# Performance work log

Hardware: AMD Instinct MI355X
Metric: run time of the kernel (lower is better)

Reference implementation:

```python
import jax, jax.numpy as jnp
import numpy as np

NUM_LEVELS = 16
MIN_RES = 16
GROWTH = 1.38
TABLE_SZ = 16384
# Per-level resolutions computed in float64 like torch's python-float b**level
RESOLUTIONS = jnp.asarray(np.floor(MIN_RES * GROWTH ** np.arange(NUM_LEVELS)).astype(np.float32))
# Spatial-hash constants; 2654435761 wraps to int32 like torch's .int() arithmetic
H2 = np.uint32(2654435761).astype(np.int32)
H3 = np.int32(805459861)
# Corner order v0..v7 from get_nearest_vertices_coords: 1 -> use ceil, 0 -> use floor
CORNERS = np.array([[0,0,0],[1,0,0],[1,1,0],[0,1,0],[0,0,1],[1,0,1],[1,1,1],[0,1,1]], dtype=bool)


def setup_inputs() -> dict:
    key = jax.random.key(0)
    kx, kt = jax.random.split(key)
    x = jax.random.uniform(kx, (262144, 3), dtype=jnp.float32)
    # original init: uniform(-1e-4, 1e-4); small-scale random values
    tables = jax.random.normal(kt, (NUM_LEVELS, TABLE_SZ, 2), dtype=jnp.float32) * 1e-4
    return {"x": x, "tables": tables}


def reference(x, tables):
    B = x.shape[0]
    F = tables.shape[-1]
    mask = jnp.asarray(CORNERS)  # [8,3]
    scaled = RESOLUTIONS[:, None, None] * x[None]        # [L,B,3]
    lo = jnp.floor(scaled).astype(jnp.int32)             # [L,B,3]
    hi = jnp.ceil(scaled).astype(jnp.int32)              # [L,B,3]
    verts = jnp.where(mask[None, None], hi[:, :, None, :], lo[:, :, None, :])  # [L,B,8,3]
    vx, vy, vz = verts[..., 0], verts[..., 1], verts[..., 2]
    # int32 spatial hash with wraparound multiply, then python-style mod (non-negative)
    idx = jnp.remainder(vx ^ (H2 * vy) ^ (H3 * vz), TABLE_SZ)  # [L,B,8]
    feats = jax.vmap(lambda t, i: t[i])(tables, idx)           # [L,B,8,F]
    # NOTE: faithful to source: interpolation weights use the UNSCALED position
    w = x - jnp.floor(x)                                       # [B,3]
    # trilinear weight per corner = prod_d (w_d if corner high else 1-w_d)
    cw = jnp.prod(jnp.where(mask[None], w[:, None, :], 1.0 - w[:, None, :]), axis=-1)  # [B,8]
    out = jnp.einsum('lbvf,bv->lbf', feats, cw)                # [L,B,F]
    return jnp.transpose(out, (1, 0, 2)).reshape(B, NUM_LEVELS * F)
```

## Files before the change

### kernel.cpp

```cpp
#include <hip/hip_runtime.h>
#include <hip/hip_fp16.h>
#include <stdint.h>


#define NUM_LEVELS 16
#define TABLE_SZ   16384
#define NCHUNK     32
#define BLOCK      512
#define TBLOCK     256

__constant__ float RESV[NUM_LEVELS] = {
    16.f, 22.f, 30.f, 42.f, 58.f, 80.f, 110.f, 152.f,
    210.f, 290.f, 400.f, 553.f, 763.f, 1053.f, 1453.f, 2005.f
};

struct PointCtx {
    uint32_t off[8];
    float    cw[8];
};

__device__ __forceinline__ void make_ctx(float px, float py, float pz, float r,
                                         PointCtx& c)
{
    float wx = px - floorf(px);
    float wy = py - floorf(py);
    float wz = pz - floorf(pz);
    float ox = 1.f - wx, oy = 1.f - wy, oz = 1.f - wz;

    c.cw[0] = ox * oy * oz;
    c.cw[1] = wx * oy * oz;
    c.cw[2] = wx * wy * oz;
    c.cw[3] = ox * wy * oz;
    c.cw[4] = ox * oy * wz;
    c.cw[5] = wx * oy * wz;
    c.cw[6] = wx * wy * wz;
    c.cw[7] = ox * wy * wz;

    float sx = r * px, sy = r * py, sz = r * pz;
    uint32_t mxl = ((uint32_t)(int)floorf(sx) & (TABLE_SZ - 1)) << 2;
    uint32_t mxh = ((uint32_t)(int)ceilf(sx)  & (TABLE_SZ - 1)) << 2;
    uint32_t myl = ((2654435761u * (uint32_t)(int)floorf(sy)) & (TABLE_SZ - 1)) << 2;
    uint32_t myh = ((2654435761u * (uint32_t)(int)ceilf(sy))  & (TABLE_SZ - 1)) << 2;
    uint32_t mzl = ((805459861u  * (uint32_t)(int)floorf(sz)) & (TABLE_SZ - 1)) << 2;
    uint32_t mzh = ((805459861u  * (uint32_t)(int)ceilf(sz))  & (TABLE_SZ - 1)) << 2;

    c.off[0] = mxl ^ myl ^ mzl;
    c.off[1] = mxh ^ myl ^ mzl;
    c.off[2] = mxh ^ myh ^ mzl;
    c.off[3] = mxl ^ myh ^ mzl;
    c.off[4] = mxl ^ myl ^ mzh;
    c.off[5] = mxh ^ myl ^ mzh;
    c.off[6] = mxh ^ myh ^ mzh;
    c.off[7] = mxl ^ myh ^ mzh;
}

template<int MODE>
__global__ __launch_bounds__(BLOCK, 4)
void hashenc_lds_kernel(const float* __restrict__ x,
                        const float* __restrict__ tables,
                        __half2* __restrict__ ws,
                        float* __restrict__ out,
                        int B, int pts_per_block)
{
    __shared__ __half2 tab[TABLE_SZ];

    const int level = blockIdx.x >> 5;
    const int chunk = blockIdx.x & (NCHUNK - 1);

    {
        const float4* __restrict__ gt4 =
            (const float4*)(tables + (size_t)level * (TABLE_SZ * 2));
        #pragma unroll
        for (int i = threadIdx.x; i < TABLE_SZ / 2; i += BLOCK) {
            float4 v = gt4[i];
            tab[2 * i]     = __floats2half2_rn(v.x, v.y);
            tab[2 * i + 1] = __floats2half2_rn(v.z, v.w);
        }
    }
    __syncthreads();

    const float r = RESV[level];
    const char* tb = (const char*)tab;
    __half2* wsl = ws + (size_t)level * B;

    int b = chunk * pts_per_block + threadIdx.x;
    const int pair_iters = pts_per_block / (2 * BLOCK);

    float pxA = x[3 * b + 0],           pyA = x[3 * b + 1],           pzA = x[3 * b + 2];
    float pxB = x[3 * (b + BLOCK) + 0], pyB = x[3 * (b + BLOCK) + 1], pzB = x[3 * (b + BLOCK) + 2];

    for (int k = 0; k < pair_iters; ++k) {
        float nxA = pxA, nyA = pyA, nzA = pzA;
        float nxB = pxB, nyB = pyB, nzB = pzB;
        int nb = b + 2 * BLOCK;
        if (k + 1 < pair_iters) {
            nxA = x[3 * nb + 0];             nyA = x[3 * nb + 1];             nzA = x[3 * nb + 2];
            nxB = x[3 * (nb + BLOCK) + 0];   nyB = x[3 * (nb + BLOCK) + 1];   nzB = x[3 * (nb + BLOCK) + 2];
        }

        PointCtx cA, cB;
        make_ctx(pxA, pyA, pzA, r, cA);
        make_ctx(pxB, pyB, pzB, r, cB);

        float2 fA[8], fB[8];
        #pragma unroll
        for (int c = 0; c < 8; ++c)
            fA[c] = __half22float2(*(const __half2*)(tb + cA.off[c]));
        #pragma unroll
        for (int c = 0; c < 8; ++c)
            fB[c] = __half22float2(*(const __half2*)(tb + cB.off[c]));

        float a0 = 0.f, a1 = 0.f, b0 = 0.f, b1 = 0.f;
        #pragma unroll
        for (int c = 0; c < 8; ++c) {
            a0 += fA[c].x * cA.cw[c];
            a1 += fA[c].y * cA.cw[c];
            b0 += fB[c].x * cB.cw[c];
            b1 += fB[c].y * cB.cw[c];
        }

        if (MODE == 0) {
            wsl[b]         = __floats2half2_rn(a0, a1);
            wsl[b + BLOCK] = __floats2half2_rn(b0, b1);
        } else {
            ((float2*)out)[(size_t)b * NUM_LEVELS + level]           = make_float2(a0, a1);
            ((float2*)out)[(size_t)(b + BLOCK) * NUM_LEVELS + level] = make_float2(b0, b1);
        }

        pxA = nxA; pyA = nyA; pzA = nzA;
        pxB = nxB; pyB = nyB; pzB = nzB;
        b = nb;
    }
}

__global__ __launch_bounds__(TBLOCK)
void transpose_kernel(const __half2* __restrict__ ws,
                      float* __restrict__ out, int B)
{
    __shared__ __half2 buf[TBLOCK][NUM_LEVELS + 1];
    const int p0 = blockIdx.x * TBLOCK;
    const int t  = threadIdx.x;

    #pragma unroll
    for (int l = 0; l < NUM_LEVELS; ++l)
        buf[t][l] = ws[(size_t)l * B + p0 + t];
    __syncthreads();

    const int pl = t >> 3;
    const int j  = t & 7;
    float4* o = (float4*)out;
    #pragma unroll
    for (int i = 0; i < 8; ++i) {
        int p = pl + i * 32;
        float2 f0 = __half22float2(buf[p][2 * j]);
        float2 f1 = __half22float2(buf[p][2 * j + 1]);
        o[(size_t)(p0 + p) * 8 + j] = make_float4(f0.x, f0.y, f1.x, f1.y);
    }
}

extern "C" void kernel_launch(void* const* d_in, const int* in_sizes, int n_in,
                              void* d_out, int out_size, void* d_ws, size_t ws_size,
                              hipStream_t stream) {
    const float* x      = (const float*)d_in[0];
    const float* tables = (const float*)d_in[1];
    float* out          = (float*)d_out;
    int B = in_sizes[0] / 3;
    int pts_per_block = (B + NCHUNK - 1) / NCHUNK;
    dim3 grid(NUM_LEVELS * NCHUNK);

    size_t ws_needed = (size_t)NUM_LEVELS * B * sizeof(__half2);
    if (ws_size >= ws_needed && (B % TBLOCK) == 0) {
        __half2* ws = (__half2*)d_ws;
        hashenc_lds_kernel<0><<<grid, BLOCK, 0, stream>>>(x, tables, ws, out, B, pts_per_block);
        transpose_kernel<<<dim3(B / TBLOCK), TBLOCK, 0, stream>>>(ws, out, B);
    } else {
        hashenc_lds_kernel<1><<<grid, BLOCK, 0, stream>>>(x, tables, nullptr, out, B, pts_per_block);
    }
}
```

Baseline: 91.95 us.

## Add prep pass converting tables to fp16 and x to SoA; async LDS fill

A new prep kernel converts the hash tables to half2 and splits x into separate x/y/z arrays once, so each of the 512 main blocks fills its LDS table with direct global-to-LDS loads of half-size data instead of loading fp32 and converting. The main loop reads coordinates with coalesced SoA loads instead of strided AoS loads, and the software prefetch of the next point pair is removed. The cost is an extra kernel launch plus workspace traffic for the converted table and the coordinates, and a stricter shape condition before falling back.

```diff
diff --git a/kernel.cpp b/kernel.cpp
--- a/kernel.cpp
+++ b/kernel.cpp
@@ -54,49 +54,69 @@
     c.off[7] = mxl ^ myh ^ mzh;
 }
 
-template<int MODE>
+__global__ __launch_bounds__(256)
+void prep_kernel(const float* __restrict__ x, const float* __restrict__ tables,
+                 __half2* __restrict__ tabf16,
+                 float* __restrict__ xs, float* __restrict__ ys,
+                 float* __restrict__ zs, int B, int entries)
+{
+    int e = blockIdx.x * 256 + threadIdx.x;
+    if (e < entries) {
+        float2 v = ((const float2*)tables)[e];
+        tabf16[e] = __floats2half2_rn(v.x, v.y);
+    }
+    if (e < B) {
+        xs[e] = x[3 * e + 0];
+        ys[e] = x[3 * e + 1];
+        zs[e] = x[3 * e + 2];
+    }
+}
+
 __global__ __launch_bounds__(BLOCK, 4)
-void hashenc_lds_kernel(const float* __restrict__ x,
-                        const float* __restrict__ tables,
-                        __half2* __restrict__ ws,
-                        float* __restrict__ out,
-                        int B, int pts_per_block)
+void pass1_kernel(const float* __restrict__ xs, const float* __restrict__ ys,
+                  const float* __restrict__ zs,
+                  const __half2* __restrict__ tabf16,
+                  __half2* __restrict__ res, int B, int pts_per_block)
 {
     __shared__ __half2 tab[TABLE_SZ];
 
     const int level = blockIdx.x >> 5;
     const int chunk = blockIdx.x & (NCHUNK - 1);
+    const int tid   = threadIdx.x;
+    const int wave  = tid >> 6;
+    const int lane  = tid & 63;
 
     {
-        const float4* __restrict__ gt4 =
-            (const float4*)(tables + (size_t)level * (TABLE_SZ * 2));
-        #pragma unroll
-        for (int i = threadIdx.x; i < TABLE_SZ / 2; i += BLOCK) {
-            float4 v = gt4[i];
-            tab[2 * i]     = __floats2half2_rn(v.x, v.y);
-            tab[2 * i + 1] = __floats2half2_rn(v.z, v.w);
+        const char* g = (const char*)(tabf16 + (size_t)level * TABLE_SZ);
+        char* s = (char*)tab;
+        const int sbase = wave * 8192;
+        #pragma unroll
+        for (int p = 0; p < 8; ++p) {
+#if __has_builtin(__builtin_amdgcn_global_load_lds)
+            __builtin_amdgcn_global_load_lds(
+                (const __attribute__((address_space(1))) void*)
+                    (g + sbase + p * 1024 + lane * 16),
+                (__attribute__((address_space(3))) void*)(s + sbase + p * 1024),
+                16, 0, 0);
+#else
+            *(float4*)(s + sbase + p * 1024 + lane * 16) =
+                *(const float4*)(g + sbase + p * 1024 + lane * 16);
+#endif
         }
     }
     __syncthreads();
 
     const float r = RESV[level];
     const char* tb = (const char*)tab;
-    __half2* wsl = ws + (size_t)level * B;
-
-    int b = chunk * pts_per_block + threadIdx.x;
+    __half2* rl = res + (size_t)level * B;
+
+    int b = chunk * pts_per_block + tid;
     const int pair_iters = pts_per_block / (2 * BLOCK);
 
-    float pxA = x[3 * b + 0],           pyA = x[3 * b + 1],           pzA = x[3 * b + 2];
-    float pxB = x[3 * (b + BLOCK) + 0], pyB = x[3 * (b + BLOCK) + 1], pzB = x[3 * (b + BLOCK) + 2];
-
     for (int k = 0; k < pair_iters; ++k) {
-        float nxA = pxA, nyA = pyA, nzA = pzA;
-        float nxB = pxB, nyB = pyB, nzB = pzB;
-        int nb = b + 2 * BLOCK;
-        if (k + 1 < pair_iters) {
-            nxA = x[3 * nb + 0];             nyA = x[3 * nb + 1];             nzA = x[3 * nb + 2];
-            nxB = x[3 * (nb + BLOCK) + 0];   nyB = x[3 * (nb + BLOCK) + 1];   nzB = x[3 * (nb + BLOCK) + 2];
-        }
+        const int bA = b, bB = b + BLOCK;
+        float pxA = xs[bA], pyA = ys[bA], pzA = zs[bA];
+        float pxB = xs[bB], pyB = ys[bB], pzB = zs[bB];
 
         PointCtx cA, cB;
         make_ctx(pxA, pyA, pzA, r, cA);
@@ -119,22 +139,15 @@
             b1 += fB[c].y * cB.cw[c];
         }
 
-        if (MODE == 0) {
-            wsl[b]         = __floats2half2_rn(a0, a1);
-            wsl[b + BLOCK] = __floats2half2_rn(b0, b1);
-        } else {
-            ((float2*)out)[(size_t)b * NUM_LEVELS + level]           = make_float2(a0, a1);
-            ((float2*)out)[(size_t)(b + BLOCK) * NUM_LEVELS + level] = make_float2(b0, b1);
-        }
-
-        pxA = nxA; pyA = nyA; pzA = nzA;
-        pxB = nxB; pyB = nyB; pzB = nzB;
-        b = nb;
+        rl[bA] = __floats2half2_rn(a0, a1);
+        rl[bB] = __floats2half2_rn(b0, b1);
+
+        b += 2 * BLOCK;
     }
 }
 
 __global__ __launch_bounds__(TBLOCK)
-void transpose_kernel(const __half2* __restrict__ ws,
+void transpose_kernel(const __half2* __restrict__ res,
                       float* __restrict__ out, int B)
 {
     __shared__ __half2 buf[TBLOCK][NUM_LEVELS + 1];
@@ -143,7 +156,7 @@
 
     #pragma unroll
     for (int l = 0; l < NUM_LEVELS; ++l)
-        buf[t][l] = ws[(size_t)l * B + p0 + t];
+        buf[t][l] = res[(size_t)l * B + p0 + t];
     __syncthreads();
 
     const int pl = t >> 3;
@@ -158,6 +171,39 @@
     }
 }
 
+__global__ __launch_bounds__(BLOCK, 4)
+void fallback_kernel(const float* __restrict__ x,
+                     const float* __restrict__ tables,
+                     float* __restrict__ out, int B, int pts_per_block)
+{
+    __shared__ __half2 tab[TABLE_SZ];
+    const int level = blockIdx.x >> 5;
+    const int chunk = blockIdx.x & (NCHUNK - 1);
+    {
+        const float4* gt4 = (const float4*)(tables + (size_t)level * (TABLE_SZ * 2));
+        for (int i = threadIdx.x; i < TABLE_SZ / 2; i += BLOCK) {
+            float4 v = gt4[i];
+            tab[2 * i]     = __floats2half2_rn(v.x, v.y);
+            tab[2 * i + 1] = __floats2half2_rn(v.z, v.w);
+        }
+    }
+    __syncthreads();
+    const float r = RESV[level];
+    const char* tb = (const char*)tab;
+    for (int b = chunk * pts_per_block + threadIdx.x;
+         b < min((chunk + 1) * pts_per_block, B); b += BLOCK) {
+        PointCtx c;
+        make_ctx(x[3 * b], x[3 * b + 1], x[3 * b + 2], r, c);
+        float a0 = 0.f, a1 = 0.f;
+        for (int i = 0; i < 8; ++i) {
+            float2 f = __half22float2(*(const __half2*)(tb + c.off[i]));
+            a0 += f.x * c.cw[i];
+            a1 += f.y * c.cw[i];
+        }
+        ((float2*)out)[(size_t)b * NUM_LEVELS + level] = make_float2(a0, a1);
+    }
+}
+
 extern "C" void kernel_launch(void* const* d_in, const int* in_sizes, int n_in,
                               void* d_out, int out_size, void* d_ws, size_t ws_size,
                               hipStream_t stream) {
@@ -165,15 +211,34 @@
     const float* tables = (const float*)d_in[1];
     float* out          = (float*)d_out;
     int B = in_sizes[0] / 3;
+    int entries = in_sizes[1] / 2;
     int pts_per_block = (B + NCHUNK - 1) / NCHUNK;
+
+    char* w = (char*)d_ws;
+    size_t off_tab = 0;
+    size_t off_xs  = off_tab + (size_t)entries * sizeof(__half2);
+    size_t off_ys  = off_xs + (size_t)B * sizeof(float);
+    size_t off_zs  = off_ys + (size_t)B * sizeof(float);
+    size_t off_res = off_zs + (size_t)B * sizeof(float);
+    size_t need    = off_res + (size_t)NUM_LEVELS * B * sizeof(__half2);
+
     dim3 grid(NUM_LEVELS * NCHUNK);
-
-    size_t ws_needed = (size_t)NUM_LEVELS * B * sizeof(__half2);
-    if (ws_size >= ws_needed && (B % TBLOCK) == 0) {
-        __half2* ws = (__half2*)d_ws;
-        hashenc_lds_kernel<0><<<grid, BLOCK, 0, stream>>>(x, tables, ws, out, B, pts_per_block);
-        transpose_kernel<<<dim3(B / TBLOCK), TBLOCK, 0, stream>>>(ws, out, B);
+    bool shape_ok = (B % (NCHUNK * 2 * BLOCK) == 0) && (B % TBLOCK == 0);
+
+    if (ws_size >= need && shape_ok) {
+        __half2* tabf16 = (__half2*)(w + off_tab);
+        float*   xs     = (float*)(w + off_xs);
+        float*   ys     = (float*)(w + off_ys);
+        float*   zs     = (float*)(w + off_zs);
+        __half2* res    = (__half2*)(w + off_res);
+
+        int pn = (B > entries ? B : entries);
+        prep_kernel<<<(pn + 255) / 256, 256, 0, stream>>>(
+            x, tables, tabf16, xs, ys, zs, B, entries);
+        pass1_kernel<<<grid, BLOCK, 0, stream>>>(
+            xs, ys, zs, tabf16, res, B, pts_per_block);
+        transpose_kernel<<<dim3(B / TBLOCK), TBLOCK, 0, stream>>>(res, out, B);
     } else {
-        hashenc_lds_kernel<1><<<grid, BLOCK, 0, stream>>>(x, tables, nullptr, out, B, pts_per_block);
-    }
-}
+        fallback_kernel<<<grid, BLOCK, 0, stream>>>(x, tables, out, B, pts_per_block);
+    }
+}
```

Result: no change. 92.40 us (+0.5%).
